# Kernel optimization log

Hardware: AMD Instinct MI355X
Metric: run time of the kernel (lower is better)

The kernel has to match this reference:

```python
import jax, jax.numpy as jnp
import numpy as np

MAX_LEN = 128
VOCAB = 32000
SENTINEL = 2**30  # larger than any valid token id; pushes masked slots to the end after sort


def setup_inputs() -> dict:
    key = jax.random.key(0)
    k1, k2, k3, k4 = jax.random.split(key, 4)
    B, L = 262144, MAX_LEN
    input_ids = jax.random.randint(k1, (B, L), 0, VOCAB, dtype=jnp.int32)
    attention_mask = jax.random.randint(k2, (B, L), 0, 2, dtype=jnp.int32)
    # MLP params: Linear(3,32) -> ReLU -> Linear(32,32) -> ReLU
    W1 = jax.random.normal(k3, (3, 32), dtype=jnp.float32) * (1.0 / np.sqrt(3.0))
    b1 = jnp.zeros((32,), dtype=jnp.float32)
    W2 = jax.random.normal(k4, (32, 32), dtype=jnp.float32) * (1.0 / np.sqrt(32.0))
    b2 = jnp.zeros((32,), dtype=jnp.float32)
    return {"input_ids": input_ids, "attention_mask": attention_mask,
            "W1": W1, "b1": b1, "W2": W2, "b2": b2}


def _symbolic_feats(input_ids, attention_mask):
    # Batched replacement of the per-row torch.unique loop:
    # sort masked tokens per row, count boundaries between distinct values.
    mask = attention_mask.astype(bool)
    seq_len = jnp.sum(mask, axis=1)  # [B]
    ids_m = jnp.where(mask, input_ids, SENTINEL)  # masked-out slots -> sentinel
    s = jnp.sort(ids_m, axis=1)  # valid tokens first (ids < SENTINEL)
    valid = s < SENTINEL
    first = jnp.ones((s.shape[0], 1), dtype=bool)
    new_val = jnp.concatenate([first, s[:, 1:] != s[:, :-1]], axis=1)
    uniq = jnp.sum(valid & new_val, axis=1)  # [B] unique count among valid tokens
    seq_f = seq_len.astype(jnp.float32)
    uniq_f = uniq.astype(jnp.float32)
    uniq_ratio = jnp.where(seq_len > 0, uniq_f / jnp.maximum(seq_f, 1.0), 0.0)
    feats = jnp.stack([seq_f / MAX_LEN, uniq_f / MAX_LEN, uniq_ratio], axis=1)  # [B,3]
    return feats


def reference(input_ids, attention_mask, W1, b1, W2, b2):
    feats = _symbolic_feats(input_ids, attention_mask)  # [B,3]
    h = jax.nn.relu(feats @ W1 + b1)
    out = jax.nn.relu(h @ W2 + b2)
    return out
```

## Files before the change

### kernel.cpp

```cpp
#include <hip/hip_runtime.h>

#define ROW_LEN 128
#define NPAIR (129 * 129)

__global__ __launch_bounds__(256) void mlp_table_kernel(
    const float* __restrict__ W1, const float* __restrict__ b1,
    const float* __restrict__ W2, const float* __restrict__ b2,
    float* __restrict__ table)
{
    const int tid = blockIdx.x * 256 + threadIdx.x;
    if (tid >= NPAIR * 32) return;
    const int p = tid >> 5;
    const int j = tid & 31;
    const int seq  = p / 129;
    const int uniq = p % 129;
    const float f0 = (float)seq  * (1.0f / 128.0f);
    const float f1 = (float)uniq * (1.0f / 128.0f);
    const float f2 = (seq > 0) ? ((float)uniq / (float)seq) : 0.0f;

    float acc = b2[j];
    #pragma unroll
    for (int jj = 0; jj < 32; ++jj) {
        float h = b1[jj];
        h = fmaf(f0, W1[jj],      h);
        h = fmaf(f1, W1[32 + jj], h);
        h = fmaf(f2, W1[64 + jj], h);
        h = fmaxf(h, 0.0f);
        acc = fmaf(h, W2[jj * 32 + j], acc);
    }
    table[tid] = fmaxf(acc, 0.0f);
}

__global__ __launch_bounds__(256, 8) void rows_kernel(
    const int* __restrict__ ids, const int* __restrict__ amask,
    const float* __restrict__ table, float* __restrict__ out, int B)
{
    __shared__ unsigned bm[4][1024];

    const int wave = threadIdx.x >> 6;
    const int lane = threadIdx.x & 63;
    const long row = (long)blockIdx.x * 4 + wave;
    if (row >= B) return;

    const long v = row * 64 + lane;
    const int2 id2 = ((const int2*)ids)[v];
    const int2 mk2 = ((const int2*)amask)[v];

    uint4* z = (uint4*)bm[wave];
    #pragma unroll
    for (int i = 0; i < 4; ++i) z[lane + i * 64] = make_uint4(0u, 0u, 0u, 0u);
    unsigned* mybm = bm[wave];

    int n0 = 0, n1 = 0;
    if (mk2.x != 0) {
        const unsigned t = (unsigned)id2.x, m = 1u << (t & 31u);
        n0 = ((atomicOr(&mybm[t >> 5], m) & m) == 0u);
    }
    if (mk2.y != 0) {
        const unsigned t = (unsigned)id2.y, m = 1u << (t & 31u);
        n1 = ((atomicOr(&mybm[t >> 5], m) & m) == 0u);
    }

    const unsigned long long s0 = __ballot(mk2.x != 0);
    const unsigned long long s1 = __ballot(mk2.y != 0);
    const unsigned long long u0 = __ballot(n0 != 0);
    const unsigned long long u1 = __ballot(n1 != 0);

    const int seq  = __popcll(s0) + __popcll(s1);
    const int uniq = __popcll(u0) + __popcll(u1);

    const int p = seq * 129 + uniq;
    if (lane < 32) out[row * 32 + lane] = table[p * 32 + lane];
}

extern "C" void kernel_launch(void* const* d_in, const int* in_sizes, int n_in,
                              void* d_out, int out_size, void* d_ws, size_t ws_size,
                              hipStream_t stream) {
    const int*   ids   = (const int*)d_in[0];
    const int*   amask = (const int*)d_in[1];
    const float* W1    = (const float*)d_in[2];
    const float* b1    = (const float*)d_in[3];
    const float* W2    = (const float*)d_in[4];
    const float* b2    = (const float*)d_in[5];
    float* out   = (float*)d_out;
    float* table = (float*)d_ws;

    const int B = in_sizes[0] / ROW_LEN;

    const int tblThreads = NPAIR * 32;
    mlp_table_kernel<<<(tblThreads + 255) / 256, 256, 0, stream>>>(W1, b1, W2, b2, table);

    rows_kernel<<<(B + 3) / 4, 256, 0, stream>>>(ids, amask, table, out, B);
}
```

Measured before the change: 282.8 us.

## Process two rows per wave with int4 loads and full-lane output writes

Each wave now handles two rows: every lane loads int4 of ids and mask, and the two rows are deduplicated one after the other with a bitmap clear in between. The gather from the table and the output write now use all 64 lanes instead of 32. This widens global loads and halves the number of blocks, but it serialises two bitmap passes per wave, adds an extra LDS clear, and leaves half the lanes idle during each pass.

```diff
diff --git a/kernel.cpp b/kernel.cpp
--- a/kernel.cpp
+++ b/kernel.cpp
@@ -31,46 +31,64 @@
     table[tid] = fmaxf(acc, 0.0f);
 }
 
+__device__ __forceinline__ int pass_row(unsigned* mybm, const int4& id,
+                                        const int4& mk, bool act)
+{
+    int s = 0, u = 0;
+    #pragma unroll
+    for (int j = 0; j < 4; ++j) {
+        const int t = (j == 0) ? id.x : (j == 1) ? id.y : (j == 2) ? id.z : id.w;
+        const int m = (j == 0) ? mk.x : (j == 1) ? mk.y : (j == 2) ? mk.z : mk.w;
+        const bool v = act && (m != 0);
+        int nw = 0;
+        if (v) {
+            const unsigned tt = (unsigned)t, bit = 1u << (tt & 31u);
+            nw = ((atomicOr(&mybm[tt >> 5], bit) & bit) == 0u);
+        }
+        s += __popcll(__ballot(v));
+        u += __popcll(__ballot(nw != 0));
+    }
+    return s * 129 + u;
+}
+
 __global__ __launch_bounds__(256, 8) void rows_kernel(
     const int* __restrict__ ids, const int* __restrict__ amask,
     const float* __restrict__ table, float* __restrict__ out, int B)
 {
     __shared__ unsigned bm[4][1024];
-
     const int wave = threadIdx.x >> 6;
     const int lane = threadIdx.x & 63;
-    const long row = (long)blockIdx.x * 4 + wave;
-    if (row >= B) return;
+    unsigned* mybm = bm[wave];
 
-    const long v = row * 64 + lane;
-    const int2 id2 = ((const int2*)ids)[v];
-    const int2 mk2 = ((const int2*)amask)[v];
+    const long rowA = ((long)blockIdx.x * 4 + wave) * 2;
+    if (rowA >= B) return;
+    const long rowL = rowA + (lane >> 5);
 
-    uint4* z = (uint4*)bm[wave];
+    const int4* ids4 = (const int4*)ids;
+    const int4* mk4v = (const int4*)amask;
+    int4 id = make_int4(0, 0, 0, 0);
+    int4 mk = make_int4(0, 0, 0, 0);
+    if (rowL < B) {
+        const long v = rowA * 32 + lane;
+        id = ids4[v];
+        mk = mk4v[v];
+    }
+
+    uint4* z = (uint4*)mybm;
     #pragma unroll
     for (int i = 0; i < 4; ++i) z[lane + i * 64] = make_uint4(0u, 0u, 0u, 0u);
-    unsigned* mybm = bm[wave];
 
-    int n0 = 0, n1 = 0;
-    if (mk2.x != 0) {
-        const unsigned t = (unsigned)id2.x, m = 1u << (t & 31u);
-        n0 = ((atomicOr(&mybm[t >> 5], m) & m) == 0u);
+    const int pA = pass_row(mybm, id, mk, lane < 32);
+
+    #pragma unroll
+    for (int i = 0; i < 4; ++i) z[lane + i * 64] = make_uint4(0u, 0u, 0u, 0u);
+
+    const int pB = pass_row(mybm, id, mk, lane >= 32);
+
+    if (rowL < B) {
+        const int p = (lane < 32) ? pA : pB;
+        out[rowA * 32 + lane] = table[p * 32 + (lane & 31)];
     }
-    if (mk2.y != 0) {
-        const unsigned t = (unsigned)id2.y, m = 1u << (t & 31u);
-        n1 = ((atomicOr(&mybm[t >> 5], m) & m) == 0u);
-    }
-
-    const unsigned long long s0 = __ballot(mk2.x != 0);
-    const unsigned long long s1 = __ballot(mk2.y != 0);
-    const unsigned long long u0 = __ballot(n0 != 0);
-    const unsigned long long u1 = __ballot(n1 != 0);
-
-    const int seq  = __popcll(s0) + __popcll(s1);
-    const int uniq = __popcll(u0) + __popcll(u1);
-
-    const int p = seq * 129 + uniq;
-    if (lane < 32) out[row * 32 + lane] = table[p * 32 + lane];
 }
 
 extern "C" void kernel_launch(void* const* d_in, const int* in_sizes, int n_in,
@@ -90,5 +108,7 @@
     const int tblThreads = NPAIR * 32;
     mlp_table_kernel<<<(tblThreads + 255) / 256, 256, 0, stream>>>(W1, b1, W2, b2, table);
 
-    rows_kernel<<<(B + 3) / 4, 256, 0, stream>>>(ids, amask, table, out, B);
+    const long pairs = ((long)B + 1) / 2;
+    const int blocks = (int)((pairs + 3) / 4);
+    rows_kernel<<<blocks, 256, 0, stream>>>(ids, amask, table, out, B);
 }
```

Result: no change. 287.7 us (+1.7%).
